# Kernel tuning notes

Hardware: AMD Instinct MI355X
Metric: run time of the kernel (lower is better)

## Reference

```python
import jax, jax.numpy as jnp
import numpy as np

C_S, C_HID, H, P, V = 128, 16, 12, 4, 8
EPS = 1e-08
SOFTPLUS_INV_1 = 0.541324854612918


def _pts_from_linear(x, n_pts):
    # torch: split [..., 3*n] into 3 chunks of n, stack on dim=-1 -> [..., n, 3]
    B, N = x.shape[:2]
    return jnp.moveaxis(x.reshape(B, N, 3, n_pts), -2, -1)


def setup_inputs() -> dict:
    key = jax.random.key(0)
    ks = jax.random.split(key, 16)
    B, N = 2, 512
    hc = H * C_HID            # 192
    hpq = H * P * 3           # 144
    hpkv = H * (P + V) * 3    # 432
    cat_dim = H * (C_HID + V * 4)  # 576
    sc = 0.02
    inp = {
        "s": jax.random.normal(ks[0], (B, N, C_S), jnp.float32),
        "R": jax.random.normal(ks[1], (B, N, 3, 3), jnp.float32),
        "t": jax.random.normal(ks[2], (B, N, 3), jnp.float32),
        "pair_mask": jnp.ones((B, N, N), jnp.float32),
        "Wq": jax.random.normal(ks[3], (C_S, hc), jnp.float32) * sc,
        "bq": jnp.zeros((hc,), jnp.float32),
        "Wkv": jax.random.normal(ks[4], (C_S, 2 * hc), jnp.float32) * sc,
        "bkv": jnp.zeros((2 * hc,), jnp.float32),
        "Wqp": jax.random.normal(ks[5], (C_S, hpq), jnp.float32) * sc,
        "bqp": jnp.zeros((hpq,), jnp.float32),
        "Wkvp": jax.random.normal(ks[6], (C_S, hpkv), jnp.float32) * sc,
        "bkvp": jnp.zeros((hpkv,), jnp.float32),
        "head_weights": jnp.full((H,), SOFTPLUS_INV_1, jnp.float32),
        "Wout": jax.random.normal(ks[7], (cat_dim, C_S), jnp.float32) * sc,
        "bout": jnp.zeros((C_S,), jnp.float32),
    }
    return inp


def reference(s, R, t, pair_mask, Wq, bq, Wkv, bkv, Wqp, bqp, Wkvp, bkvp,
              head_weights, Wout, bout):
    B, N, _ = s.shape
    # scalar q/k/v
    q = (s @ Wq + bq).reshape(B, N, H, C_HID)
    kv = (s @ Wkv + bkv).reshape(B, N, H, 2 * C_HID)
    k, v = kv[..., :C_HID], kv[..., C_HID:]

    # point q/k/v in global frame: R x + t
    qp = _pts_from_linear(s @ Wqp + bqp, H * P)           # [B,N,HP,3]
    qp = jnp.einsum('bnij,bnpj->bnpi', R, qp) + t[:, :, None]
    qp = qp.reshape(B, N, H, P, 3)
    kvp = _pts_from_linear(s @ Wkvp + bkvp, H * (P + V))  # [B,N,H(P+V),3]
    kvp = jnp.einsum('bnij,bnpj->bnpi', R, kvp) + t[:, :, None]
    kvp = kvp.reshape(B, N, H, P + V, 3)
    kp, vp = kvp[..., :P, :], kvp[..., P:, :]

    # scalar attention logits [B,H,N,N]
    a = jnp.einsum('bihc,bjhc->bhij', q, k) * (1.0 / np.sqrt(3 * C_HID))

    # point-distance bias: sum_p ||q_i - k_j||^2 via |q|^2+|k|^2-2q.k
    sq_q = jnp.sum(qp * qp, axis=(-1, -2))   # [B,N,H]
    sq_k = jnp.sum(kp * kp, axis=(-1, -2))   # [B,N,H]
    cross = jnp.einsum('bihpc,bjhpc->bhij', qp, kp)
    d2 = (jnp.swapaxes(sq_q, 1, 2)[..., :, None]
          + jnp.swapaxes(sq_k, 1, 2)[..., None, :]
          - 2.0 * cross)                      # [B,H,N,N]
    hw = jax.nn.softplus(head_weights) * np.sqrt(1.0 / (3 * (P * 9.0 / 2)))
    pt_att = d2 * hw[None, :, None, None] * (-0.5)

    square_mask = 100000.0 * (pair_mask - 1.0)            # [B,N,N]
    a = jax.nn.softmax(a + pt_att + square_mask[:, None], axis=-1)

    # scalar output
    o = jnp.einsum('bhij,bjhc->bihc', a, v).reshape(B, N, H * C_HID)

    # point output, rotated back to local frame: R^T (x - t) form -> R^T x - t
    o_pt = jnp.einsum('bhij,bjhvc->bihvc', a, vp)         # [B,N,H,V,3]
    o_pt = jnp.einsum('bnji,bnhvj->bnhvi', R, o_pt) - t[:, :, None, None]
    o_pt_norm = jnp.sqrt(jnp.sum(o_pt * o_pt, axis=-1) + EPS).reshape(B, N, H * V)
    o_pt_flat = o_pt.reshape(B, N, H * V, 3)

    cat = jnp.concatenate(
        [o, o_pt_flat[..., 0], o_pt_flat[..., 1], o_pt_flat[..., 2], o_pt_norm],
        axis=-1)                                           # [B,N,576]
    return cat @ Wout + bout
```

## Files before the change

kernel.cpp:

```cpp
#include <hip/hip_runtime.h>
#include <hip/hip_bf16.h>
#include <math.h>

#define H_    12
#define B_    2
#define N_    512
#define BH_   (B_*H_)
#define QSCALE 0.14433756729740643f
#define CPT_K  0.13608276348795434f

#define OFF_QB   1356928
#define OFF_KP   1553536
#define OFF_VP   1750144
#define OFF_SA   2045056
#define OFF_SB   2057344
#define OFF_CATP 2069632

typedef __attribute__((ext_vector_type(8))) short sh8;
typedef __attribute__((ext_vector_type(4))) float f32x4;
typedef unsigned short u16t;

static __device__ __forceinline__ u16t f2b(float x) {
    __hip_bfloat16 h = __float2bfloat16(x);
    return *reinterpret_cast<u16t*>(&h);
}
static __device__ __forceinline__ int catp_idx(int tok, int col) {
    return (tok >> 4)*9216 + (col >> 5)*512 + ((col >> 3) & 3)*128
         + (tok & 15)*8 + (col & 7);
}

__global__ __launch_bounds__(512) void projpack_kernel(
    const float* __restrict__ s,
    const float* __restrict__ Rg, const float* __restrict__ tg,
    const float* __restrict__ hwg,
    const float* __restrict__ Wq,  const float* __restrict__ bq,
    const float* __restrict__ Wkv, const float* __restrict__ bkv,
    const float* __restrict__ Wqp, const float* __restrict__ bqp,
    const float* __restrict__ Wkvp,const float* __restrict__ bkvp,
    float* __restrict__ ws)
{
    __shared__ float ldsP[8][1160];

    u16t* Qb = (u16t*)(ws + OFF_QB);
    u16t* Kp = (u16t*)(ws + OFF_KP);
    u16t* Vp = (u16t*)(ws + OFF_VP);
    float* sa_g = ws + OFF_SA;
    float* sb_g = ws + OFF_SB;

    const int tid  = threadIdx.x;
    const int w    = tid >> 6, lane = tid & 63;
    const int kq   = lane >> 4, lx = lane & 15;
    const int half = blockIdx.x & 1;
    const int tok0 = (blockIdx.x >> 1) * 8;
    const int b    = tok0 >> 9, n0 = tok0 & 511;

    sh8 afr[4];
    #pragma unroll
    for (int ks = 0; ks < 4; ++ks) {
        const float* src = s + (tok0 + (lx & 7))*128 + ks*32 + kq*8;
        float4 u0 = *(const float4*)(src);
        float4 u1 = *(const float4*)(src+4);
        union { sh8 v; u16t u[8]; } pk;
        pk.u[0]=f2b(u0.x); pk.u[1]=f2b(u0.y); pk.u[2]=f2b(u0.z); pk.u[3]=f2b(u0.w);
        pk.u[4]=f2b(u1.x); pk.u[5]=f2b(u1.y); pk.u[6]=f2b(u1.z); pk.u[7]=f2b(u1.w);
        afr[ks] = pk.v;
    }

    const int gstart = (w < 4) ? w*5 : 20 + (w-4)*4;
    const int ng     = (w < 4) ? 5 : 4;

    for (int g = 0; g < ng; ++g) {
        int gg  = half*36 + gstart + g;
        int col = gg*16 + lx;
        const float* wsrc; int lc, od; float bv;
        if (col < 192)      { wsrc = Wq;   lc = col;     od = 192; bv = bq[lc]; }
        else if (col < 576) { wsrc = Wkv;  lc = col-192; od = 384; bv = bkv[lc]; }
        else if (col < 720) { wsrc = Wqp;  lc = col-576; od = 144; bv = bqp[lc]; }
        else                { wsrc = Wkvp; lc = col-720; od = 432; bv = bkvp[lc]; }

        f32x4 acc = {0.f,0.f,0.f,0.f};
        #pragma unroll
        for (int ks = 0; ks < 4; ++ks) {
            int k0 = ks*32 + kq*8;
            union { sh8 v; u16t u[8]; } pk;
            #pragma unroll
            for (int j = 0; j < 8; ++j) pk.u[j] = f2b(wsrc[(k0+j)*od + lc]);
            acc = __builtin_amdgcn_mfma_f32_16x16x32_bf16(afr[ks], pk.v, acc, 0, 0, 0);
        }
        if (kq < 2) {
            #pragma unroll
            for (int r = 0; r < 4; ++r)
                ldsP[kq*4 + r][gg*16 + lx] = acc[r] + bv;
        }
    }
    __syncthreads();

    if (half == 1) {
        for (int idx = tid; idx < 8*48; idx += 512) {
            int tk = idx / 48, p = idx % 48;
            int tok = tok0 + tk;
            const float* Rr = Rg + tok*9;
            const float* tr = tg + tok*3;
            float x0 = ldsP[tk][576 +  0 + p];
            float x1 = ldsP[tk][576 + 48 + p];
            float x2 = ldsP[tk][576 + 96 + p];
            ldsP[tk][576 +  0 + p] = Rr[0]*x0 + Rr[1]*x1 + Rr[2]*x2 + tr[0];
            ldsP[tk][576 + 48 + p] = Rr[3]*x0 + Rr[4]*x1 + Rr[5]*x2 + tr[1];
            ldsP[tk][576 + 96 + p] = Rr[6]*x0 + Rr[7]*x1 + Rr[8]*x2 + tr[2];
        }
        for (int idx = tid; idx < 8*144; idx += 512) {
            int tk = idx / 144, p = idx % 144;
            int tok = tok0 + tk;
            const float* Rr = Rg + tok*9;
            const float* tr = tg + tok*3;
            float x0 = ldsP[tk][720 +   0 + p];
            float x1 = ldsP[tk][720 + 144 + p];
            float x2 = ldsP[tk][720 + 288 + p];
            ldsP[tk][720 +   0 + p] = Rr[0]*x0 + Rr[1]*x1 + Rr[2]*x2 + tr[0];
            ldsP[tk][720 + 144 + p] = Rr[3]*x0 + Rr[4]*x1 + Rr[5]*x2 + tr[1];
            ldsP[tk][720 + 288 + p] = Rr[6]*x0 + Rr[7]*x1 + Rr[8]*x2 + tr[2];
        }
        __syncthreads();

        for (int idx = tid; idx < 8*12; idx += 512) {
            int tk = idx / 12, h = idx % 12;
            float hx = hwg[h];
            float sp = (hx > 20.f) ? hx : log1pf(__expf(hx));
            float qs = sp * CPT_K;
            union { sh8 v[2]; u16t u[16]; } pk;
            #pragma unroll
            for (int e = 0; e < 12; ++e)
                pk.u[e] = f2b(ldsP[tk][576 + (e%3)*48 + h*4 + e/3] * qs);
            pk.u[12]=0; pk.u[13]=0; pk.u[14]=0; pk.u[15]=0;
            u16t* dst = Qb + ((b*H_+h)*N_ + n0 + tk)*32 + 16;
            *(sh8*)dst = pk.v[0];
            *(sh8*)(dst+8) = pk.v[1];
        }
        for (int idx = tid; idx < 8*24; idx += 512) {
            int tk = idx / 24, r2 = idx % 24, h = r2 >> 1, fq = 2 + (r2 & 1);
            int j = n0 + tk, bh = b*H_ + h;
            union { sh8 v; u16t u[8]; } pk;
            #pragma unroll
            for (int e = 0; e < 8; ++e) {
                int c = fq*8 + e;
                float val;
                if (c < 28) val = ldsP[tk][720 + ((c-16)%3)*144 + h*12 + (c-16)/3];
                else        val = 0.f;
                pk.u[e] = f2b(val);
            }
            *(sh8*)(Kp + bh*16384 + (j>>4)*512 + fq*128 + (j&15)*8) = pk.v;
        }
        for (int idx = tid; idx < 12*24; idx += 512) {
            int h = idx / 24, d = 16 + idx % 24;
            int bh = b*H_ + h;
            union { sh8 v; u16t u[8]; } pk;
            #pragma unroll
            for (int e = 0; e < 8; ++e)
                pk.u[e] = f2b(ldsP[e][720 + ((d-16)%3)*144 + h*12 + 4 + (d-16)/3]);
            int j = n0;
            *(sh8*)(Vp + bh*24576 + (j>>5)*1536 + (d>>4)*512 + ((j>>3)&3)*128
                    + (d&15)*8) = pk.v;
        }
        for (int idx = tid; idx < 8*12; idx += 512) {
            int tk = idx / 12, h = idx % 12;
            float hx = hwg[h];
            float sp = (hx > 20.f) ? hx : log1pf(__expf(hx));
            float c_pt = -0.5f * sp * CPT_K;
            float sq = 0.f, sk = 0.f;
            #pragma unroll
            for (int pp = 0; pp < 4; ++pp)
                #pragma unroll
                for (int c = 0; c < 3; ++c) {
                    float a = ldsP[tk][576 + c*48  + h*4  + pp]; sq += a*a;
                    float k = ldsP[tk][720 + c*144 + h*12 + pp]; sk += k*k;
                }
            sa_g[(b*H_+h)*N_ + n0 + tk] = c_pt * sq;
            sb_g[(b*H_+h)*N_ + n0 + tk] = c_pt * sk;
        }
    } else {
        for (int idx = tid; idx < 8*12; idx += 512) {
            int tk = idx / 12, h = idx % 12;
            union { sh8 v[2]; u16t u[16]; } pk;
            #pragma unroll
            for (int e = 0; e < 16; ++e) pk.u[e] = f2b(ldsP[tk][h*16 + e] * QSCALE);
            u16t* dst = Qb + ((b*H_+h)*N_ + n0 + tk)*32;
            *(sh8*)dst = pk.v[0];
            *(sh8*)(dst+8) = pk.v[1];
        }
        for (int idx = tid; idx < 8*24; idx += 512) {
            int tk = idx / 24, r2 = idx % 24, h = r2 >> 1, fq = r2 & 1;
            int j = n0 + tk, bh = b*H_ + h;
            union { sh8 v; u16t u[8]; } pk;
            #pragma unroll
            for (int e = 0; e < 8; ++e)
                pk.u[e] = f2b(ldsP[tk][192 + h*32 + fq*8 + e]);
            *(sh8*)(Kp + bh*16384 + (j>>4)*512 + fq*128 + (j&15)*8) = pk.v;
        }
        for (int idx = tid; idx < 12*16; idx += 512) {
            int h = idx / 16, d = idx % 16;
            int bh = b*H_ + h;
            union { sh8 v; u16t u[8]; } pk;
            #pragma unroll
            for (int e = 0; e < 8; ++e)
                pk.u[e] = f2b(ldsP[e][192 + h*32 + 16 + d]);
            int j = n0;
            *(sh8*)(Vp + bh*24576 + (j>>5)*1536 + (d>>4)*512 + ((j>>3)&3)*128
                    + (d&15)*8) = pk.v;
        }
    }
}

__global__ __launch_bounds__(512, 2) void attn_kernel(
    const float* __restrict__ Rg, const float* __restrict__ tg,
    const float* __restrict__ maskg, float* __restrict__ ws)
{
    __shared__ u16t smP[8*16*72];
    __shared__ float mbuf[3*128*20];
    __shared__ float obuf[32*32];

    const u16t* Qb = (const u16t*)(ws + OFF_QB);
    const u16t* Kp = (const u16t*)(ws + OFF_KP);
    const u16t* Vp = (const u16t*)(ws + OFF_VP);
    const float* sa_g = ws + OFF_SA;
    const float* sb_g = ws + OFF_SB;
    u16t* catp = (u16t*)(ws + OFF_CATP);

    const int tid  = threadIdx.x;
    const int w    = tid >> 6, lane = tid & 63;
    const int rg   = w & 1, jh = w >> 1;
    const int kq   = lane >> 4, lx = lane & 15;
    const int bh   = blockIdx.x >> 4;
    const int it   = blockIdx.x & 15;
    const int b    = bh / H_, h = bh % H_;
    const int i0   = it * 32;

    sh8 qfrag = *(const sh8*)(Qb + (bh*N_ + i0 + rg*16 + lx)*32 + kq*8);
    float sa_r[4];
    #pragma unroll
    for (int r = 0; r < 4; ++r)
        sa_r[r] = sa_g[bh*N_ + i0 + rg*16 + kq*4 + r];

    float m_run[4] = {-1e30f,-1e30f,-1e30f,-1e30f};
    float l_run[4] = {0.f,0.f,0.f,0.f};
    f32x4 oc0 = {0.f,0.f,0.f,0.f}, oc1 = oc0, oc2 = oc0;

    const float* mrow = maskg + (size_t)(b*N_ + i0 + rg*16 + kq*4)*N_ + lx;
    u16t* pw = smP + w*1152;

    #pragma unroll
    for (int t = 0; t < 2; ++t) {
        const int jt = jh*2 + t;
        const int j0 = jt * 64;

        f32x4 sc[4];
        #pragma unroll
        for (int st = 0; st < 4; ++st) {
            sh8 kf = *(const sh8*)(Kp + bh*16384 + (jt*4+st)*512 + kq*128 + lx*8);
            f32x4 z = {0.f,0.f,0.f,0.f};
            sc[st] = __builtin_amdgcn_mfma_f32_16x16x32_bf16(qfrag, kf, z, 0, 0, 0);
        }
        float sbv[4];
        #pragma unroll
        for (int st = 0; st < 4; ++st) sbv[st] = sb_g[bh*N_ + j0 + st*16 + lx];
        float mb[16];
        #pragma unroll
        for (int r = 0; r < 4; ++r)
            #pragma unroll
            for (int st = 0; st < 4; ++st)
                mb[r*4+st] = mrow[r*N_ + j0 + st*16];

        float L[16];
        #pragma unroll
        for (int st = 0; st < 4; ++st)
            #pragma unroll
            for (int r = 0; r < 4; ++r)
                L[st*4+r] = sc[st][r] + sa_r[r] + sbv[st] + 1e5f*(mb[r*4+st] - 1.f);

        #pragma unroll
        for (int r = 0; r < 4; ++r) {
            float tm = fmaxf(fmaxf(L[0*4+r], L[1*4+r]), fmaxf(L[2*4+r], L[3*4+r]));
            tm = fmaxf(tm, __shfl_xor(tm, 1));
            tm = fmaxf(tm, __shfl_xor(tm, 2));
            tm = fmaxf(tm, __shfl_xor(tm, 4));
            tm = fmaxf(tm, __shfl_xor(tm, 8));
            float mnew = fmaxf(m_run[r], tm);
            float al = __expf(m_run[r] - mnew);
            m_run[r] = mnew;
            l_run[r] *= al;
            oc0[r] *= al; oc1[r] *= al; oc2[r] *= al;
        }
        #pragma unroll
        for (int st = 0; st < 4; ++st)
            #pragma unroll
            for (int r = 0; r < 4; ++r) {
                float p = __expf(L[st*4+r] - m_run[r]);
                l_run[r] += p;
                pw[(kq*4+r)*72 + st*16 + lx] = f2b(p);
            }
        #pragma unroll
        for (int c = 0; c < 2; ++c) {
            sh8 pa = *(const sh8*)(pw + lx*72 + c*32 + kq*8);
            #pragma unroll
            for (int nq = 0; nq < 3; ++nq) {
                sh8 vf = *(const sh8*)(Vp + bh*24576 + (jt*2+c)*1536 + nq*512
                                        + kq*128 + lx*8);
                if (nq == 0) oc0 = __builtin_amdgcn_mfma_f32_16x16x32_bf16(pa, vf, oc0, 0,0,0);
                if (nq == 1) oc1 = __builtin_amdgcn_mfma_f32_16x16x32_bf16(pa, vf, oc1, 0,0,0);
                if (nq == 2) oc2 = __builtin_amdgcn_mfma_f32_16x16x32_bf16(pa, vf, oc2, 0,0,0);
            }
        }
    }

    if (jh > 0) {
        float* mb = mbuf + ((jh-1)*128 + rg*64 + lane)*20;
        #pragma unroll
        for (int r = 0; r < 4; ++r) {
            mb[r]      = m_run[r];
            mb[4 + r]  = l_run[r];
            mb[8 + r]  = oc0[r];
            mb[12 + r] = oc1[r];
            mb[16 + r] = oc2[r];
        }
    }
    __syncthreads();
    if (jh == 0) {
        float linv[4];
        #pragma unroll
        for (int r = 0; r < 4; ++r) {
            float ms = m_run[r];
            #pragma unroll
            for (int q = 0; q < 3; ++q)
                ms = fmaxf(ms, mbuf[(q*128 + rg*64 + lane)*20 + r]);
            float eA = __expf(m_run[r] - ms);
            float l = l_run[r]*eA;
            oc0[r] *= eA; oc1[r] *= eA; oc2[r] *= eA;
            #pragma unroll
            for (int q = 0; q < 3; ++q) {
                const float* mb = mbuf + (q*128 + rg*64 + lane)*20;
                float e = __expf(mb[r] - ms);
                l      += mb[4+r]*e;
                oc0[r] += mb[8+r]*e;
                oc1[r] += mb[12+r]*e;
                oc2[r] += mb[16+r]*e;
            }
            l += __shfl_xor(l, 1); l += __shfl_xor(l, 2);
            l += __shfl_xor(l, 4); l += __shfl_xor(l, 8);
            linv[r] = 1.f / l;
        }

        #pragma unroll
        for (int r = 0; r < 4; ++r) {
            int tok = b*N_ + i0 + rg*16 + kq*4 + r;
            catp[catp_idx(tok, h*16 + lx)] = f2b(oc0[r] * linv[r]);
            obuf[(rg*16 + kq*4 + r)*32 + lx]      = oc1[r] * linv[r];
            obuf[(rg*16 + kq*4 + r)*32 + 16 + lx] = oc2[r] * linv[r];
        }

        #pragma unroll
        for (int tsk = 0; tsk < 2; ++tsk) {
            int task = lane + tsk*64;
            int r = task >> 3, pv = task & 7;
            int tok = b*N_ + i0 + rg*16 + r;
            const float* Rr = Rg + tok*9;
            const float* tr = tg + tok*3;
            float g0 = obuf[(rg*16 + r)*32 + pv*3 + 0];
            float g1 = obuf[(rg*16 + r)*32 + pv*3 + 1];
            float g2 = obuf[(rg*16 + r)*32 + pv*3 + 2];
            float px = Rr[0]*g0 + Rr[3]*g1 + Rr[6]*g2 - tr[0];
            float py = Rr[1]*g0 + Rr[4]*g1 + Rr[7]*g2 - tr[1];
            float pz = Rr[2]*g0 + Rr[5]*g1 + Rr[8]*g2 - tr[2];
            float nrm = sqrtf(px*px + py*py + pz*pz + 1e-8f);
            catp[catp_idx(tok, 192 + h*8 + pv)] = f2b(px);
            catp[catp_idx(tok, 288 + h*8 + pv)] = f2b(py);
            catp[catp_idx(tok, 384 + h*8 + pv)] = f2b(pz);
            catp[catp_idx(tok, 480 + h*8 + pv)] = f2b(nrm);
        }
    }
}

__global__ __launch_bounds__(512) void out_kernel(
    const float* __restrict__ Wout, const float* __restrict__ bout,
    const float* __restrict__ ws, float* __restrict__ out)
{
    __shared__ float part[2][3][64][4];

    const int tid = threadIdx.x;
    const int w = tid >> 6, lane = tid & 63;
    const int cg = w & 1, kh = w >> 1;
    const int lx = lane & 15, kq = lane >> 4;
    const int nt = blockIdx.x, mt = blockIdx.y;

    const sh8* Ap = (const sh8*)((const u16t*)(ws + OFF_CATP));

    const int col = nt*32 + cg*16 + lx;
    const int ke0 = (kh*18) >> 2;
    const int ke1 = ((kh+1)*18) >> 2;

    f32x4 acc = {0.f,0.f,0.f,0.f};
    #pragma unroll 5
    for (int ks = ke0; ks < ke1; ++ks) {
        sh8 af = Ap[((mt*18 + ks)*4 + kq)*16 + lx];
        int k0 = ks*32 + kq*8;
        union { sh8 v; u16t u[8]; } pk;
        #pragma unroll
        for (int j = 0; j < 8; ++j) pk.u[j] = f2b(Wout[(k0+j)*128 + col]);
        acc = __builtin_amdgcn_mfma_f32_16x16x32_bf16(af, pk.v, acc, 0, 0, 0);
    }
    if (kh > 0) {
        #pragma unroll
        for (int r = 0; r < 4; ++r) part[cg][kh-1][lane][r] = acc[r];
    }
    __syncthreads();
    if (kh == 0) {
        float bv = bout[col];
        #pragma unroll
        for (int r = 0; r < 4; ++r) {
            int row = mt*16 + kq*4 + r;
            out[row*128 + col] = acc[r] + part[cg][0][lane][r]
                               + part[cg][1][lane][r] + part[cg][2][lane][r] + bv;
        }
    }
}

extern "C" void kernel_launch(void* const* d_in, const int* in_sizes, int n_in,
                              void* d_out, int out_size, void* d_ws, size_t ws_size,
                              hipStream_t stream) {
    const float* s    = (const float*)d_in[0];
    const float* R    = (const float*)d_in[1];
    const float* t    = (const float*)d_in[2];
    const float* mask = (const float*)d_in[3];
    const float* Wq   = (const float*)d_in[4];
    const float* bq   = (const float*)d_in[5];
    const float* Wkv  = (const float*)d_in[6];
    const float* bkv  = (const float*)d_in[7];
    const float* Wqp  = (const float*)d_in[8];
    const float* bqp  = (const float*)d_in[9];
    const float* Wkvp = (const float*)d_in[10];
    const float* bkvp = (const float*)d_in[11];
    const float* hw   = (const float*)d_in[12];
    const float* Wout = (const float*)d_in[13];
    const float* bout = (const float*)d_in[14];
    float* ws  = (float*)d_ws;
    float* out = (float*)d_out;

    projpack_kernel<<<256, 512, 0, stream>>>(s, R, t, hw, Wq, bq, Wkv, bkv,
                                             Wqp, bqp, Wkvp, bkvp, ws);
    attn_kernel<<<BH_*16, 512, 0, stream>>>(R, t, mask, ws);
    out_kernel<<<dim3(4, 64), 512, 0, stream>>>(Wout, bout, ws, out);
}
```

Before: 108.4 us.

## Fuse output projection into attention kernel via per-head partial GEMM and atomics

```diff
diff --git a/kernel.cpp b/kernel.cpp
--- a/kernel.cpp
+++ b/kernel.cpp
@@ -14,7 +14,6 @@
 #define OFF_VP   1750144
 #define OFF_SA   2045056
 #define OFF_SB   2057344
-#define OFF_CATP 2069632
 
 typedef __attribute__((ext_vector_type(8))) short sh8;
 typedef __attribute__((ext_vector_type(4))) float f32x4;
@@ -23,10 +22,6 @@
 static __device__ __forceinline__ u16t f2b(float x) {
     __hip_bfloat16 h = __float2bfloat16(x);
     return *reinterpret_cast<u16t*>(&h);
-}
-static __device__ __forceinline__ int catp_idx(int tok, int col) {
-    return (tok >> 4)*9216 + (col >> 5)*512 + ((col >> 3) & 3)*128
-         + (tok & 15)*8 + (col & 7);
 }
 
 __global__ __launch_bounds__(512) void projpack_kernel(
@@ -37,7 +32,8 @@
     const float* __restrict__ Wkv, const float* __restrict__ bkv,
     const float* __restrict__ Wqp, const float* __restrict__ bqp,
     const float* __restrict__ Wkvp,const float* __restrict__ bkvp,
-    float* __restrict__ ws)
+    const float* __restrict__ bout,
+    float* __restrict__ ws, float* __restrict__ out)
 {
     __shared__ float ldsP[8][1160];
 
@@ -207,23 +203,29 @@
             *(sh8*)(Vp + bh*24576 + (j>>5)*1536 + (d>>4)*512 + ((j>>3)&3)*128
                     + (d&15)*8) = pk.v;
         }
+        for (int idx = tid; idx < 8*128; idx += 512) {
+            int tk = idx >> 7, c = idx & 127;
+            out[(tok0 + tk)*128 + c] = bout[c];
+        }
     }
 }
 
 __global__ __launch_bounds__(512, 2) void attn_kernel(
     const float* __restrict__ Rg, const float* __restrict__ tg,
-    const float* __restrict__ maskg, float* __restrict__ ws)
+    const float* __restrict__ maskg, const float* __restrict__ Woutg,
+    float* __restrict__ ws, float* __restrict__ out)
 {
-    __shared__ u16t smP[8*16*72];
-    __shared__ float mbuf[3*128*20];
-    __shared__ float obuf[32*32];
+    __shared__ __align__(16) char ldsraw[49152];
+    u16t*  smP  = (u16t*)ldsraw;
+    float* obuf = (float*)ldsraw;
+    float* ldsC = (float*)(ldsraw + 4096);
+    float* mbuf = (float*)(ldsraw + 18432);
 
     const u16t* Qb = (const u16t*)(ws + OFF_QB);
     const u16t* Kp = (const u16t*)(ws + OFF_KP);
     const u16t* Vp = (const u16t*)(ws + OFF_VP);
     const float* sa_g = ws + OFF_SA;
     const float* sb_g = ws + OFF_SB;
-    u16t* catp = (u16t*)(ws + OFF_CATP);
 
     const int tid  = threadIdx.x;
     const int w    = tid >> 6, lane = tid & 63;
@@ -350,74 +352,67 @@
 
         #pragma unroll
         for (int r = 0; r < 4; ++r) {
-            int tok = b*N_ + i0 + rg*16 + kq*4 + r;
-            catp[catp_idx(tok, h*16 + lx)] = f2b(oc0[r] * linv[r]);
-            obuf[(rg*16 + kq*4 + r)*32 + lx]      = oc1[r] * linv[r];
-            obuf[(rg*16 + kq*4 + r)*32 + 16 + lx] = oc2[r] * linv[r];
+            int row = rg*16 + kq*4 + r;
+            ldsC[row*52 + lx] = oc0[r] * linv[r];
+            obuf[row*32 + lx]      = oc1[r] * linv[r];
+            obuf[row*32 + 16 + lx] = oc2[r] * linv[r];
         }
 
         #pragma unroll
         for (int tsk = 0; tsk < 2; ++tsk) {
             int task = lane + tsk*64;
             int r = task >> 3, pv = task & 7;
-            int tok = b*N_ + i0 + rg*16 + r;
+            int row = rg*16 + r;
+            int tok = b*N_ + i0 + row;
             const float* Rr = Rg + tok*9;
             const float* tr = tg + tok*3;
-            float g0 = obuf[(rg*16 + r)*32 + pv*3 + 0];
-            float g1 = obuf[(rg*16 + r)*32 + pv*3 + 1];
-            float g2 = obuf[(rg*16 + r)*32 + pv*3 + 2];
+            float g0 = obuf[row*32 + pv*3 + 0];
+            float g1 = obuf[row*32 + pv*3 + 1];
+            float g2 = obuf[row*32 + pv*3 + 2];
             float px = Rr[0]*g0 + Rr[3]*g1 + Rr[6]*g2 - tr[0];
             float py = Rr[1]*g0 + Rr[4]*g1 + Rr[7]*g2 - tr[1];
             float pz = Rr[2]*g0 + Rr[5]*g1 + Rr[8]*g2 - tr[2];
             float nrm = sqrtf(px*px + py*py + pz*pz + 1e-8f);
-            catp[catp_idx(tok, 192 + h*8 + pv)] = f2b(px);
-            catp[catp_idx(tok, 288 + h*8 + pv)] = f2b(py);
-            catp[catp_idx(tok, 384 + h*8 + pv)] = f2b(pz);
-            catp[catp_idx(tok, 480 + h*8 + pv)] = f2b(nrm);
-        }
-    }
-}
-
-__global__ __launch_bounds__(512) void out_kernel(
-    const float* __restrict__ Wout, const float* __restrict__ bout,
-    const float* __restrict__ ws, float* __restrict__ out)
-{
-    __shared__ float part[2][3][64][4];
-
-    const int tid = threadIdx.x;
-    const int w = tid >> 6, lane = tid & 63;
-    const int cg = w & 1, kh = w >> 1;
-    const int lx = lane & 15, kq = lane >> 4;
-    const int nt = blockIdx.x, mt = blockIdx.y;
-
-    const sh8* Ap = (const sh8*)((const u16t*)(ws + OFF_CATP));
-
-    const int col = nt*32 + cg*16 + lx;
-    const int ke0 = (kh*18) >> 2;
-    const int ke1 = ((kh+1)*18) >> 2;
-
-    f32x4 acc = {0.f,0.f,0.f,0.f};
-    #pragma unroll 5
-    for (int ks = ke0; ks < ke1; ++ks) {
-        sh8 af = Ap[((mt*18 + ks)*4 + kq)*16 + lx];
-        int k0 = ks*32 + kq*8;
-        union { sh8 v; u16t u[8]; } pk;
-        #pragma unroll
-        for (int j = 0; j < 8; ++j) pk.u[j] = f2b(Wout[(k0+j)*128 + col]);
-        acc = __builtin_amdgcn_mfma_f32_16x16x32_bf16(af, pk.v, acc, 0, 0, 0);
-    }
-    if (kh > 0) {
-        #pragma unroll
-        for (int r = 0; r < 4; ++r) part[cg][kh-1][lane][r] = acc[r];
+            ldsC[row*52 + 16 + pv] = px;
+            ldsC[row*52 + 24 + pv] = py;
+            ldsC[row*52 + 32 + pv] = pz;
+            ldsC[row*52 + 40 + pv] = nrm;
+        }
     }
     __syncthreads();
-    if (kh == 0) {
-        float bv = bout[col];
-        #pragma unroll
-        for (int r = 0; r < 4; ++r) {
-            int row = mt*16 + kq*4 + r;
-            out[row*128 + col] = acc[r] + part[cg][0][lane][r]
-                               + part[cg][1][lane][r] + part[cg][2][lane][r] + bv;
+
+    {
+        const int ncol = w*16 + lx;
+        auto wrow = [h](int kk) -> int {
+            return (kk < 16) ? (h*16 + kk)
+                             : (192 + ((kk-16) >> 3)*96 + h*8 + ((kk-16) & 7));
+        };
+        union { sh8 v; u16t u[8]; } bf0, bf1;
+        #pragma unroll
+        for (int j = 0; j < 8; ++j) {
+            int k0 = kq*8 + j;
+            bf0.u[j] = f2b(Woutg[wrow(k0)*128 + ncol]);
+            int k1 = 32 + kq*8 + j;
+            bf1.u[j] = (k1 < 48) ? f2b(Woutg[wrow(k1)*128 + ncol]) : (u16t)0;
+        }
+        #pragma unroll
+        for (int m = 0; m < 2; ++m) {
+            union { sh8 v; u16t u[8]; } af0, af1;
+            const float* crow = ldsC + (m*16 + lx)*52;
+            #pragma unroll
+            for (int j = 0; j < 8; ++j) {
+                af0.u[j] = f2b(crow[kq*8 + j]);
+                int k1 = 32 + kq*8 + j;
+                af1.u[j] = (k1 < 48) ? f2b(crow[k1]) : (u16t)0;
+            }
+            f32x4 acc = {0.f,0.f,0.f,0.f};
+            acc = __builtin_amdgcn_mfma_f32_16x16x32_bf16(af0.v, bf0.v, acc, 0, 0, 0);
+            acc = __builtin_amdgcn_mfma_f32_16x16x32_bf16(af1.v, bf1.v, acc, 0, 0, 0);
+            #pragma unroll
+            for (int r = 0; r < 4; ++r) {
+                int row = b*N_ + i0 + m*16 + kq*4 + r;
+                atomicAdd(&out[row*128 + ncol], acc[r]);
+            }
         }
     }
 }
@@ -444,7 +439,6 @@
     float* out = (float*)d_out;
 
     projpack_kernel<<<256, 512, 0, stream>>>(s, R, t, hw, Wq, bq, Wkv, bkv,
-                                             Wqp, bqp, Wkvp, bkvp, ws);
-    attn_kernel<<<BH_*16, 512, 0, stream>>>(R, t, mask, ws);
-    out_kernel<<<dim3(4, 64), 512, 0, stream>>>(Wout, bout, ws, out);
+                                             Wqp, bqp, Wkvp, bkvp, bout, ws, out);
+    attn_kernel<<<BH_*16, 512, 0, stream>>>(R, t, mask, Wout, ws, out);
 }
```

Measured after the change: 110.3 us. No clear change (+1.8%).
